# Performance work log

Measured on AMD Instinct MI355X. Metric: run time of the kernel, lower is better.

## Reference

```python
import jax, jax.numpy as jnp
import numpy as np

H = 128          # hidden_dim
OUT = 128        # output_dim
NB = 8           # num_bilinear
NS = 7           # num_spherical
NR = 6           # num_radial
N_BEFORE = 1
N_AFTER = 2
E = 50000        # num_edges
T = 200000       # num_triplets


def _lin_init(key, fan_in, fan_out):
    return jax.random.normal(key, (fan_in, fan_out), jnp.float32) / jnp.sqrt(jnp.float32(fan_in))


def setup_inputs() -> dict:
    key = jax.random.key(0)
    ks = jax.random.split(key, 24)
    inp = {
        "x": jax.random.normal(ks[0], (E, H), jnp.float32),
        "rbf": jax.random.normal(ks[1], (E, NR), jnp.float32),
        "sbf": jax.random.normal(ks[2], (T, NS * NR), jnp.float32),
        "idx_kj": jax.random.randint(ks[3], (T,), 0, E),
        "idx_ji": jax.random.randint(ks[4], (T,), 0, E),
        # params (weights stored [in, out]; y = x @ W + b)
        "W_rbf": _lin_init(ks[5], NR, H),
        "W_sbf": _lin_init(ks[6], NS * NR, NB),
        "Wkj": _lin_init(ks[7], H, H), "bkj": jnp.zeros((H,), jnp.float32),
        "Wji": _lin_init(ks[8], H, H), "bji": jnp.zeros((H,), jnp.float32),
        "Wbil": jax.random.normal(ks[9], (H, NB, H), jnp.float32) * (2.0 / H),
        "before_W1": jax.random.normal(ks[10], (N_BEFORE, H, H), jnp.float32) / jnp.sqrt(jnp.float32(H)),
        "before_b1": jnp.zeros((N_BEFORE, H), jnp.float32),
        "before_W2": jax.random.normal(ks[11], (N_BEFORE, H, H), jnp.float32) / jnp.sqrt(jnp.float32(H)),
        "before_b2": jnp.zeros((N_BEFORE, H), jnp.float32),
        "Wlin": _lin_init(ks[12], H, H), "blin": jnp.zeros((H,), jnp.float32),
        "after_W1": jax.random.normal(ks[13], (N_AFTER, H, H), jnp.float32) / jnp.sqrt(jnp.float32(H)),
        "after_b1": jnp.zeros((N_AFTER, H), jnp.float32),
        "after_W2": jax.random.normal(ks[14], (N_AFTER, H, H), jnp.float32) / jnp.sqrt(jnp.float32(H)),
        "after_b2": jnp.zeros((N_AFTER, H), jnp.float32),
        "Wout": _lin_init(ks[15], H, OUT), "bout": jnp.zeros((OUT,), jnp.float32),
    }
    return inp


def _fwd(x, rbf, sbf, W_rbf, W_sbf, Wkj, bkj, Wji, bji, Wbil,
         before_W1, before_b1, before_W2, before_b2, Wlin, blin,
         after_W1, after_b1, after_W2, after_b2, Wout, bout,
         idx_kj, idx_ji):
    act = jax.nn.silu  # swish
    rbf_h = rbf @ W_rbf                       # [E, H]
    sbf_h = sbf @ W_sbf                       # [T, NB]
    x_ji = act(x @ Wji + bji)                 # [E, H]
    x_kj = act(x @ Wkj + bkj) * rbf_h         # [E, H]
    xg = x_kj[idx_kj]                         # gather -> [T, H]
    # bilinear: out[w,i] = sum_{j,l} sbf_h[w,j] * xg[w,l] * Wbil[i,j,l]
    # loop over the small num_bilinear axis to avoid a [T,H,NB] intermediate
    msg = sbf_h[:, 0:1] * (xg @ Wbil[:, 0, :].T)
    for j in range(1, NB):
        msg = msg + sbf_h[:, j:j + 1] * (xg @ Wbil[:, j, :].T)
    agg = jax.ops.segment_sum(msg, idx_ji, num_segments=x.shape[0])  # scatter-sum [E, H]
    h = x_ji + agg
    for i in range(before_W1.shape[0]):
        h = h + act(act(h @ before_W1[i] + before_b1[i]) @ before_W2[i] + before_b2[i])
    h = act(h @ Wlin + blin) + x
    for i in range(after_W1.shape[0]):
        h = h + act(act(h @ after_W1[i] + after_b1[i]) @ after_W2[i] + after_b2[i])
    return act(h @ Wout + bout)


def reference(x, rbf, sbf, idx_kj, idx_ji, W_rbf, W_sbf, Wkj, bkj, Wji, bji, Wbil,
              before_W1, before_b1, before_W2, before_b2, Wlin, blin,
              after_W1, after_b1, after_W2, after_b2, Wout, bout):
    return _fwd(x, rbf, sbf, W_rbf, W_sbf, Wkj, bkj, Wji, bji, Wbil,
                before_W1, before_b1, before_W2, before_b2, Wlin, blin,
                after_W1, after_b1, after_W2, after_b2, Wout, bout,
                idx_kj, idx_ji)
```

## Files before the change

### kernel.cpp

```cpp
#include <hip/hip_runtime.h>
#include <hip/hip_bf16.h>

#define NEDGE 50000
#define NTRI 200000

typedef __attribute__((ext_vector_type(8))) short short8;
typedef __attribute__((ext_vector_type(4))) short short4v;
typedef __attribute__((ext_vector_type(4))) float f32x4;

__device__ __forceinline__ float silu_f(float v) { return v / (1.0f + __expf(-v)); }

__device__ __forceinline__ short f2bf(float f) {
    unsigned u = __float_as_uint(f);
    unsigned r = (u + 0x7FFFu + ((u >> 16) & 1u)) >> 16;
    return (short)r;
}
__device__ __forceinline__ float bf2f(short s) {
    return __uint_as_float(((unsigned)(unsigned short)s) << 16);
}


__global__ void cvt_kernel(const float* __restrict__ src, short* __restrict__ dst, int n4) {
    int i = blockIdx.x * 256 + threadIdx.x;
    if (i < n4) {
        float4 v = ((const float4*)src)[i];
        short4v o;
        o[0] = f2bf(v.x); o[1] = f2bf(v.y); o[2] = f2bf(v.z); o[3] = f2bf(v.w);
        ((short4v*)dst)[i] = o;
    }
}

struct TP { const float* s[10]; short* d[10]; };
__global__ void t128_all(TP p) {
    const float* __restrict__ src = p.s[blockIdx.y];
    short* __restrict__ dst = p.d[blockIdx.y];
    int i = blockIdx.x * 256 + threadIdx.x;
    int k = i >> 7, n = i & 127;
    dst[n * 128 + k] = f2bf(src[i]);
}

__global__ __launch_bounds__(256) void sbfh_kernel(const float* __restrict__ sbf,
                                                   const float* __restrict__ Wsbf,
                                                   float* __restrict__ out) {
    __shared__ float s[32 * 42];
    __shared__ float w[42 * 8];
    int tid = threadIdx.x;
    size_t base = (size_t)blockIdx.x * 32;
    for (int u = tid; u < 32 * 42; u += 256) s[u] = sbf[base * 42 + u];
    for (int u = tid; u < 42 * 8; u += 256) w[u] = Wsbf[u];
    __syncthreads();
    int row = tid >> 3, j = tid & 7;
    float acc = 0.f;
    #pragma unroll
    for (int k = 0; k < 42; ++k) acc += s[row * 42 + k] * w[k * 8 + j];
    out[base * 8 + tid] = acc;
}


__global__ void hist_kernel(const int* __restrict__ ji, int* __restrict__ counts) {
    int i = blockIdx.x * 256 + threadIdx.x;
    if (i < NTRI) atomicAdd(&counts[ji[i]], 1);
}

__global__ void scan1_kernel(const int* __restrict__ counts, int* __restrict__ partial,
                             int* __restrict__ bsum) {
    __shared__ int tmp[256];
    int tid = threadIdx.x;
    int i = blockIdx.x * 256 + tid;
    int v = (i < NEDGE) ? counts[i] : 0;
    tmp[tid] = v; __syncthreads();
    #pragma unroll
    for (int o = 1; o < 256; o <<= 1) {
        int t = (tid >= o) ? tmp[tid - o] : 0;
        __syncthreads();
        tmp[tid] += t;
        __syncthreads();
    }
    if (i < NEDGE) partial[i] = tmp[tid] - v;
    if (tid == 255) bsum[blockIdx.x] = tmp[255];
}

__global__ void scan2_kernel(int* __restrict__ bsum, int nb) {
    __shared__ int tmp[256];
    int tid = threadIdx.x;
    int v = (tid < nb) ? bsum[tid] : 0;
    tmp[tid] = v; __syncthreads();
    #pragma unroll
    for (int o = 1; o < 256; o <<= 1) {
        int t = (tid >= o) ? tmp[tid - o] : 0;
        __syncthreads();
        tmp[tid] += t;
        __syncthreads();
    }
    if (tid < nb) bsum[tid] = tmp[tid] - v;
}

__global__ void scan3_kernel(const int* __restrict__ partial, const int* __restrict__ bsum,
                             int* __restrict__ rowptr, int* __restrict__ wcur) {
    int i = blockIdx.x * 256 + threadIdx.x;
    if (i < NEDGE) {
        int r = partial[i] + bsum[blockIdx.x];
        rowptr[i] = r;
        wcur[i] = r;
    }
}

__global__ void scatter_kernel(const int* __restrict__ ji, int* __restrict__ wcur,
                               int* __restrict__ perm) {
    int w = blockIdx.x * 256 + threadIdx.x;
    if (w < NTRI) {
        int p = atomicAdd(&wcur[ji[w]], 1);
        perm[p] = w;
    }
}

__global__ void permute_kernel(const int* __restrict__ perm, const int* __restrict__ idx_kj,
                               const float* __restrict__ sbfh, int* __restrict__ kjp,
                               float* __restrict__ sbfhp) {
    int p = blockIdx.x * 256 + threadIdx.x;
    if (p < NTRI) {
        int w = perm[p];
        kjp[p] = idx_kj[w];
        float4 a = *(const float4*)(sbfh + (size_t)w * 8);
        float4 b = *(const float4*)(sbfh + (size_t)w * 8 + 4);
        *(float4*)(sbfhp + (size_t)p * 8) = a;
        *(float4*)(sbfhp + (size_t)p * 8 + 4) = b;
    }
}

#define BE 32
__global__ __launch_bounds__(512) void bilinear_fused(
    const short* __restrict__ xkj, const float* __restrict__ sbfhp,
    const int* __restrict__ kjp, const int* __restrict__ rowptr,
    const int* __restrict__ counts,
    const float* __restrict__ xji, const short* __restrict__ WbT,
    float* __restrict__ h, short* __restrict__ hb)
{
    __shared__ __align__(16) short ylds[BE * 1024];
    __shared__ __align__(16) short blds[128 * 64];

    int tid = threadIdx.x;
    int e0 = blockIdx.x * BE;
    int wv = tid >> 6, lane = tid & 63, g = lane >> 4, ln = lane & 15;

    int eidx = e0 + ((lane < BE) ? lane : BE - 1);
    if (eidx > NEDGE - 1) eidx = NEDGE - 1;
    int rp_l = rowptr[eidx];
    int ct_l = counts[eidx];

    for (int es = 0; es < 4; ++es) {
        int e_loc = wv * 4 + es;
        int e = e0 + e_loc;
        float accA[8], accB[8];
        #pragma unroll
        for (int j = 0; j < 8; ++j) { accA[j] = 0.f; accB[j] = 0.f; }
        if (e < NEDGE) {
            int p0 = __builtin_amdgcn_readfirstlane(__shfl(rp_l, e_loc));
            int n  = __builtin_amdgcn_readfirstlane(__shfl(ct_l, e_loc));
            for (int tc = 0; tc < n; tc += 64) {
                int mm = n - tc; if (mm > 64) mm = 64;
                int li = (lane < mm) ? lane : mm - 1;
                int kt = kjp[p0 + tc + li];
                for (int tb = 0; tb < mm; tb += 4) {
                    int m4 = mm - tb; if (m4 > 4) m4 = 4;
                    int i1 = tb + 1 < mm ? tb + 1 : mm - 1;
                    int i2 = tb + 2 < mm ? tb + 2 : mm - 1;
                    int i3 = tb + 3 < mm ? tb + 3 : mm - 1;
                    int k0 = __shfl(kt, tb), k1 = __shfl(kt, i1);
                    int k2 = __shfl(kt, i2), k3 = __shfl(kt, i3);
                    unsigned xv0 = *(const unsigned*)(xkj + (size_t)k0 * 128 + lane * 2);
                    unsigned xv1 = *(const unsigned*)(xkj + (size_t)k1 * 128 + lane * 2);
                    unsigned xv2 = *(const unsigned*)(xkj + (size_t)k2 * 128 + lane * 2);
                    unsigned xv3 = *(const unsigned*)(xkj + (size_t)k3 * 128 + lane * 2);
                    unsigned xq[4] = {xv0, xv1, xv2, xv3};
                    #pragma unroll
                    for (int s = 0; s < 4; ++s) {
                        if (s < m4) {
                            float x0 = bf2f((short)(xq[s] & 0xffff));
                            float x1 = bf2f((short)(xq[s] >> 16));
                            const float* sp = sbfhp + (size_t)(p0 + tc + tb + s) * 8;
                            #pragma unroll
                            for (int j = 0; j < 8; ++j) {
                                float sv = sp[j];
                                accA[j] += sv * x0; accB[j] += sv * x1;
                            }
                        }
                    }
                }
            }
        }
        unsigned xr = (unsigned)((e_loc & 7) << 4);
        #pragma unroll
        for (int j = 0; j < 8; ++j) {
            unsigned bo = ((unsigned)(e_loc * 2048 + (j * 256 + lane * 4))) ^ xr;
            unsigned pk = (unsigned)(unsigned short)f2bf(accA[j]) |
                          ((unsigned)(unsigned short)f2bf(accB[j]) << 16);
            *(unsigned*)((char*)ylds + bo) = pk;
        }
    }

    int rt = wv >> 2, cq = wv & 3;
    f32x4 acc0 = (f32x4){0.f,0.f,0.f,0.f}, acc1 = (f32x4){0.f,0.f,0.f,0.f};

    short8 wreg0, wreg1;
    {
        int u0 = tid, u1 = tid + 512;
        wreg0 = *(const short8*)(WbT + (size_t)(u0 >> 3) * 1024 + (u0 & 7) * 8);
        wreg1 = *(const short8*)(WbT + (size_t)(u1 >> 3) * 1024 + (u1 & 7) * 8);
    }

    for (int c = 0; c < 16; ++c) {
        __syncthreads();
        {
            int u0 = tid, u1 = tid + 512;
            int bi0 = u0 >> 3, bc0 = u0 & 7;
            int bi1 = u1 >> 3, bc1 = u1 & 7;
            unsigned bo0 = (unsigned)(bi0 * 128 + bc0 * 16) ^ (unsigned)((bi0 & 7) << 4);
            unsigned bo1 = (unsigned)(bi1 * 128 + bc1 * 16) ^ (unsigned)((bi1 & 7) << 4);
            *(short8*)((char*)blds + bo0) = wreg0;
            *(short8*)((char*)blds + bo1) = wreg1;
            if (c < 15) {
                wreg0 = *(const short8*)(WbT + (size_t)bi0 * 1024 + (c + 1) * 64 + bc0 * 8);
                wreg1 = *(const short8*)(WbT + (size_t)bi1 * 1024 + (c + 1) * 64 + bc1 * 8);
            }
        }
        __syncthreads();
        #pragma unroll
        for (int kk = 0; kk < 2; ++kk) {
            int row = rt * 16 + ln;
            unsigned ab = ((unsigned)(row * 2048 + (c * 64 + kk * 32 + g * 8) * 2))
                          ^ ((unsigned)((row & 7) << 4));
            short8 a = *(short8*)((char*)ylds + ab);
            #pragma unroll
            for (int nt = 0; nt < 2; ++nt) {
                int bi = cq * 32 + nt * 16 + ln;
                unsigned bb = ((unsigned)(bi * 128 + kk * 64 + g * 16))
                              ^ ((unsigned)((bi & 7) << 4));
                short8 b = *(short8*)((char*)blds + bb);
                if (nt == 0) acc0 = __builtin_amdgcn_mfma_f32_16x16x32_bf16(a, b, acc0, 0, 0, 0);
                else         acc1 = __builtin_amdgcn_mfma_f32_16x16x32_bf16(a, b, acc1, 0, 0, 0);
            }
        }
    }

    #pragma unroll
    for (int nt = 0; nt < 2; ++nt) {
        int col = cq * 32 + nt * 16 + ln;
        #pragma unroll
        for (int r2 = 0; r2 < 4; ++r2) {
            int e = e0 + rt * 16 + g * 4 + r2;
            if (e < NEDGE) {
                size_t o = (size_t)e * 128 + col;
                float v = (nt == 0 ? acc0[r2] : acc1[r2]) + xji[o];
                h[o] = v; hb[o] = f2bf(v);
            }
        }
    }
}

__global__ __launch_bounds__(256) void gemm_x(
    const short* __restrict__ xb, const short* __restrict__ Wjit,
    const short* __restrict__ Wkjt, const float* __restrict__ bji,
    const float* __restrict__ bkj, const float* __restrict__ rbf,
    const float* __restrict__ Wrbf, float* __restrict__ xji,
    short* __restrict__ xkj)
{
    __shared__ __align__(16) short w1[128 * 128];
    __shared__ __align__(16) short w2[128 * 128];
    int tid = threadIdx.x;
    int wv = tid >> 6, lane = tid & 63, g = lane >> 4, ln = lane & 15;
    int rowBase = blockIdx.x * 64 + wv * 16;

    #pragma unroll
    for (int q = 0; q < 8; ++q) {
        int idx = tid + q * 256;
        int wi = idx >> 4, wc = idx & 15;
        unsigned bo = (unsigned)(wi * 256 + wc * 16) ^ (unsigned)((wi & 7) << 4);
        *(short8*)((char*)w1 + bo) = *(const short8*)(Wjit + wi * 128 + wc * 8);
        *(short8*)((char*)w2 + bo) = *(const short8*)(Wkjt + wi * 128 + wc * 8);
    }

    int arow = rowBase + ln; if (arow > NEDGE - 1) arow = NEDGE - 1;
    const short8* Ar = (const short8*)(xb + (size_t)arow * 128);
    short8 af[4];
    #pragma unroll
    for (int kc = 0; kc < 4; ++kc) af[kc] = Ar[kc * 4 + g];

    __syncthreads();

    f32x4 acc1[8], acc2[8];
    #pragma unroll
    for (int nt = 0; nt < 8; ++nt) {
        acc1[nt] = (f32x4){0.f,0.f,0.f,0.f};
        acc2[nt] = (f32x4){0.f,0.f,0.f,0.f};
    }
    #pragma unroll
    for (int kc = 0; kc < 4; ++kc) {
        #pragma unroll
        for (int nt = 0; nt < 8; ++nt) {
            int wi = nt * 16 + ln;
            unsigned bo = (unsigned)(wi * 256 + kc * 64 + g * 16) ^ (unsigned)((wi & 7) << 4);
            short8 b1 = *(short8*)((char*)w1 + bo);
            short8 b2 = *(short8*)((char*)w2 + bo);
            acc1[nt] = __builtin_amdgcn_mfma_f32_16x16x32_bf16(af[kc], b1, acc1[nt], 0, 0, 0);
            acc2[nt] = __builtin_amdgcn_mfma_f32_16x16x32_bf16(af[kc], b2, acc2[nt], 0, 0, 0);
        }
    }

    #pragma unroll
    for (int r = 0; r < 4; ++r) {
        int row = rowBase + g * 4 + r;
        bool ok = row < NEDGE;
        int crow = ok ? row : NEDGE - 1;
        float rr[6];
        #pragma unroll
        for (int q = 0; q < 6; ++q) rr[q] = rbf[(size_t)crow * 6 + q];
        #pragma unroll
        for (int nt = 0; nt < 8; ++nt) {
            int col = nt * 16 + ln;
            if (ok) {
                size_t o = (size_t)row * 128 + col;
                xji[o] = silu_f(acc1[nt][r] + bji[col]);
                float rb = 0.f;
                #pragma unroll
                for (int q = 0; q < 6; ++q) rb += rr[q] * Wrbf[q * 128 + col];
                xkj[o] = f2bf(silu_f(acc2[nt][r] + bkj[col]) * rb);
            }
        }
    }
}

struct ChainP { const short* W[8]; const float* B[8]; };
__global__ __launch_bounds__(256) void chain_kernel(
    ChainP p, const short* __restrict__ hb, const float* __restrict__ hin,
    const float* __restrict__ x, float* __restrict__ out)
{
    __shared__ __align__(16) short wlds[2][128 * 128];
    __shared__ __align__(16) short actlds[64 * 128];
    int tid = threadIdx.x;
    int wv = tid >> 6, lane = tid & 63, g = lane >> 4, ln = lane & 15;
    int rowBase = blockIdx.x * 64;

    #pragma unroll
    for (int q = 0; q < 8; ++q) {
        int idx = tid + q * 256;
        int wi = idx >> 4, wc = idx & 15;
        unsigned bo = (unsigned)(wi * 256 + wc * 16) ^ (unsigned)((wi & 7) << 4);
        *(short8*)((char*)wlds[0] + bo) = *(const short8*)(p.W[0] + wi * 128 + wc * 8);
    }

    float hreg[8][4];
    #pragma unroll
    for (int nt = 0; nt < 8; ++nt)
        #pragma unroll
        for (int r = 0; r < 4; ++r) {
            int row = rowBase + wv * 16 + g * 4 + r;
            if (row > NEDGE - 1) row = NEDGE - 1;
            hreg[nt][r] = hin[(size_t)row * 128 + nt * 16 + ln];
        }

    int arow = rowBase + wv * 16 + ln; if (arow > NEDGE - 1) arow = NEDGE - 1;
    short8 af[4];
    #pragma unroll
    for (int kc = 0; kc < 4; ++kc)
        af[kc] = *(const short8*)(hb + (size_t)arow * 128 + kc * 32 + g * 8);

    const int modes[8] = {0, 1, 2, 0, 1, 0, 1, 3};

    #pragma unroll
    for (int l = 0; l < 8; ++l) {
        __syncthreads();
        if (l > 0) {
            int ar = wv * 16 + ln;
            unsigned sw = ((unsigned)(ar & 7)) << 4;
            #pragma unroll
            for (int kc = 0; kc < 4; ++kc)
                af[kc] = *(short8*)((char*)actlds +
                          (((unsigned)(ar * 256 + (kc * 32 + g * 8) * 2)) ^ sw));
        }
        __syncthreads();

        f32x4 acc[8];
        #pragma unroll
        for (int nt = 0; nt < 8; ++nt) acc[nt] = (f32x4){0.f,0.f,0.f,0.f};
        #pragma unroll
        for (int kc = 0; kc < 4; ++kc) {
            #pragma unroll
            for (int nt = 0; nt < 8; ++nt) {
                int wi = nt * 16 + ln;
                unsigned bo = (unsigned)(wi * 256 + kc * 64 + g * 16) ^ (unsigned)((wi & 7) << 4);
                short8 b = *(short8*)((char*)wlds[l & 1] + bo);
                acc[nt] = __builtin_amdgcn_mfma_f32_16x16x32_bf16(af[kc], b, acc[nt], 0, 0, 0);
            }
        }

        if (l < 7) {
            #pragma unroll
            for (int q = 0; q < 8; ++q) {
                int idx = tid + q * 256;
                int wi = idx >> 4, wc = idx & 15;
                unsigned bo = (unsigned)(wi * 256 + wc * 16) ^ (unsigned)((wi & 7) << 4);
                *(short8*)((char*)wlds[(l + 1) & 1] + bo) =
                    *(const short8*)(p.W[l + 1] + wi * 128 + wc * 8);
            }
        }

        int mode = modes[l];
        #pragma unroll
        for (int nt = 0; nt < 8; ++nt) {
            int col = nt * 16 + ln;
            float bv = p.B[l][col];
            #pragma unroll
            for (int r = 0; r < 4; ++r) {
                int lrow = wv * 16 + g * 4 + r;
                int row = rowBase + lrow;
                float v = silu_f(acc[nt][r] + bv);
                if (mode == 1) { v += hreg[nt][r]; hreg[nt][r] = v; }
                else if (mode == 2) {
                    int cr = row > NEDGE - 1 ? NEDGE - 1 : row;
                    v += x[(size_t)cr * 128 + col];
                    hreg[nt][r] = v;
                } else if (mode == 3) {
                    if (row < NEDGE) out[(size_t)row * 128 + col] = v;
                }
                if (mode != 3) {
                    unsigned sw2 = ((unsigned)(lrow & 7)) << 4;
                    unsigned bo = ((unsigned)(lrow * 256 + col * 2)) ^ sw2;
                    *(short*)((char*)actlds + bo) = f2bf(v);
                }
            }
        }
    }
}

extern "C" void kernel_launch(void* const* d_in, const int* in_sizes, int n_in,
                              void* d_out, int out_size, void* d_ws, size_t ws_size,
                              hipStream_t stream) {
    const float* x      = (const float*)d_in[0];
    const float* rbf    = (const float*)d_in[1];
    const float* sbf    = (const float*)d_in[2];
    const int*   idx_kj = (const int*)d_in[3];
    const int*   idx_ji = (const int*)d_in[4];
    const float* W_rbf  = (const float*)d_in[5];
    const float* W_sbf  = (const float*)d_in[6];
    const float* Wkj    = (const float*)d_in[7];
    const float* bkj    = (const float*)d_in[8];
    const float* Wji    = (const float*)d_in[9];
    const float* bji    = (const float*)d_in[10];
    const float* Wbil   = (const float*)d_in[11];
    const float* bW1    = (const float*)d_in[12];
    const float* bb1    = (const float*)d_in[13];
    const float* bW2    = (const float*)d_in[14];
    const float* bb2    = (const float*)d_in[15];
    const float* Wlin   = (const float*)d_in[16];
    const float* blin   = (const float*)d_in[17];
    const float* aW1    = (const float*)d_in[18];
    const float* ab1    = (const float*)d_in[19];
    const float* aW2    = (const float*)d_in[20];
    const float* ab2    = (const float*)d_in[21];
    const float* Wout   = (const float*)d_in[22];
    const float* bout   = (const float*)d_in[23];
    float* out = (float*)d_out;

    char* ws = (char*)d_ws;
    size_t off = 0;
    auto alloc = [&](size_t bytes) { char* p = ws + off; off += bytes; return p; };
    short* xb    = (short*)alloc((size_t)NEDGE * 128 * 2);
    short* xkj   = (short*)alloc((size_t)NEDGE * 128 * 2);
    short* hbb   = (short*)alloc((size_t)NEDGE * 128 * 2);
    float* sbfh  = (float*)alloc((size_t)NTRI * 8 * 4);
    float* sbfhp = (float*)alloc(((size_t)NTRI * 8 + 64) * 4);
    float* xji   = (float*)alloc((size_t)NEDGE * 128 * 4);
    float* h     = (float*)alloc((size_t)NEDGE * 128 * 4);
    short* WbT   = (short*)alloc((size_t)131072 * 2);
    short* Wt[10];
    for (int i = 0; i < 10; ++i) Wt[i] = (short*)alloc((size_t)16384 * 2);
    int* counts  = (int*)alloc((size_t)NEDGE * 4);
    int* partial = (int*)alloc((size_t)NEDGE * 4);
    int* rowptr  = (int*)alloc((size_t)NEDGE * 4);
    int* wcur    = (int*)alloc((size_t)NEDGE * 4);
    int* bsum    = (int*)alloc(256 * 4);
    int* perm    = (int*)alloc((size_t)NTRI * 4);
    int* kjp     = (int*)alloc((size_t)(NTRI + 64) * 4);
    (void)ws_size; (void)n_in; (void)in_sizes; (void)out_size;

    hipMemsetAsync(counts, 0, (size_t)NEDGE * 4, stream);

    cvt_kernel<<<dim3((NEDGE * 128 / 4 + 255) / 256), 256, 0, stream>>>(x, xb, NEDGE * 128 / 4);
    cvt_kernel<<<dim3((131072 / 4 + 255) / 256), 256, 0, stream>>>(Wbil, WbT, 131072 / 4);

    TP tp;
    const float* srcs[10] = {Wkj, Wji, bW1, bW2, Wlin, aW1, aW1 + 16384, aW2, aW2 + 16384, Wout};
    for (int i = 0; i < 10; ++i) { tp.s[i] = srcs[i]; tp.d[i] = Wt[i]; }
    t128_all<<<dim3(64, 10), 256, 0, stream>>>(tp);

    sbfh_kernel<<<dim3(NTRI / 32), 256, 0, stream>>>(sbf, W_sbf, sbfh);

    int NB1 = (NEDGE + 255) / 256;
    hist_kernel<<<dim3((NTRI + 255) / 256), 256, 0, stream>>>(idx_ji, counts);
    scan1_kernel<<<dim3(NB1), 256, 0, stream>>>(counts, partial, bsum);
    scan2_kernel<<<dim3(1), 256, 0, stream>>>(bsum, NB1);
    scan3_kernel<<<dim3(NB1), 256, 0, stream>>>(partial, bsum, rowptr, wcur);
    scatter_kernel<<<dim3((NTRI + 255) / 256), 256, 0, stream>>>(idx_ji, wcur, perm);
    permute_kernel<<<dim3((NTRI + 255) / 256), 256, 0, stream>>>(perm, idx_kj, sbfh, kjp, sbfhp);

    int gE = (NEDGE + 63) / 64;
    gemm_x<<<gE, 256, 0, stream>>>(xb, Wt[1], Wt[0], bji, bkj, rbf, W_rbf, xji, xkj);

    bilinear_fused<<<dim3((NEDGE + BE - 1) / BE), 512, 0, stream>>>(
        xkj, sbfhp, kjp, rowptr, counts, xji, WbT, h, hbb);

    ChainP cp;
    cp.W[0] = Wt[2]; cp.B[0] = bb1;
    cp.W[1] = Wt[3]; cp.B[1] = bb2;
    cp.W[2] = Wt[4]; cp.B[2] = blin;
    cp.W[3] = Wt[5]; cp.B[3] = ab1;
    cp.W[4] = Wt[7]; cp.B[4] = ab2;
    cp.W[5] = Wt[6]; cp.B[5] = ab1 + 128;
    cp.W[6] = Wt[8]; cp.B[6] = ab2 + 128;
    cp.W[7] = Wt[9]; cp.B[7] = bout;
    chain_kernel<<<gE, 256, 0, stream>>>(cp, hbb, h, x, out);
}
```

Baseline: 357.7 us.

## Fuse scatter with permute and split chain kernel columns across twice the waves

Merges the scatter and permute kernels so each triplet writes its kj index and sbf_h row straight into its CSR slot, which drops the perm array and one launch. The chain kernel now runs 512 threads, with two waves sharing each 16-row tile and each wave computing half the output columns. It keeps a single LDS weight buffer, prefetching the next layer's weights into registers and writing them to LDS after the barrier. It also initialises the accumulators with the bias and packs bf16 pairs with a lane shuffle into 32-bit LDS stores. The aims are more waves per CU, less LDS use, and fewer kernel launches, at the cost of a less coalesced scattered write of sbf_h and extra register pressure from the prefetched weights.

```diff
diff --git a/kernel.cpp b/kernel.cpp
--- a/kernel.cpp
+++ b/kernel.cpp
@@ -105,21 +105,12 @@
     }
 }
 
-__global__ void scatter_kernel(const int* __restrict__ ji, int* __restrict__ wcur,
-                               int* __restrict__ perm) {
+__global__ void scatter_kernel(const int* __restrict__ ji, const int* __restrict__ idx_kj,
+                               const float* __restrict__ sbfh, int* __restrict__ wcur,
+                               int* __restrict__ kjp, float* __restrict__ sbfhp) {
     int w = blockIdx.x * 256 + threadIdx.x;
     if (w < NTRI) {
         int p = atomicAdd(&wcur[ji[w]], 1);
-        perm[p] = w;
-    }
-}
-
-__global__ void permute_kernel(const int* __restrict__ perm, const int* __restrict__ idx_kj,
-                               const float* __restrict__ sbfh, int* __restrict__ kjp,
-                               float* __restrict__ sbfhp) {
-    int p = blockIdx.x * 256 + threadIdx.x;
-    if (p < NTRI) {
-        int w = perm[p];
         kjp[p] = idx_kj[w];
         float4 a = *(const float4*)(sbfh + (size_t)w * 8);
         float4 b = *(const float4*)(sbfh + (size_t)w * 8 + 4);
@@ -331,47 +322,56 @@
 }
 
 struct ChainP { const short* W[8]; const float* B[8]; };
-__global__ __launch_bounds__(256) void chain_kernel(
+__global__ __launch_bounds__(512, 4) void chain_kernel(
     ChainP p, const short* __restrict__ hb, const float* __restrict__ hin,
     const float* __restrict__ x, float* __restrict__ out)
 {
-    __shared__ __align__(16) short wlds[2][128 * 128];
+    __shared__ __align__(16) short wlds[128 * 128];
     __shared__ __align__(16) short actlds[64 * 128];
     int tid = threadIdx.x;
     int wv = tid >> 6, lane = tid & 63, g = lane >> 4, ln = lane & 15;
+    int rt = wv >> 1, ch = wv & 1;
     int rowBase = blockIdx.x * 64;
 
     #pragma unroll
-    for (int q = 0; q < 8; ++q) {
-        int idx = tid + q * 256;
+    for (int q = 0; q < 4; ++q) {
+        int idx = tid + q * 512;
         int wi = idx >> 4, wc = idx & 15;
         unsigned bo = (unsigned)(wi * 256 + wc * 16) ^ (unsigned)((wi & 7) << 4);
-        *(short8*)((char*)wlds[0] + bo) = *(const short8*)(p.W[0] + wi * 128 + wc * 8);
-    }
-
-    float hreg[8][4];
-    #pragma unroll
-    for (int nt = 0; nt < 8; ++nt)
+        *(short8*)((char*)wlds + bo) = *(const short8*)(p.W[0] + wi * 128 + wc * 8);
+    }
+
+    float hreg[4][4];
+    #pragma unroll
+    for (int nt = 0; nt < 4; ++nt)
         #pragma unroll
         for (int r = 0; r < 4; ++r) {
-            int row = rowBase + wv * 16 + g * 4 + r;
+            int row = rowBase + rt * 16 + g * 4 + r;
             if (row > NEDGE - 1) row = NEDGE - 1;
-            hreg[nt][r] = hin[(size_t)row * 128 + nt * 16 + ln];
-        }
-
-    int arow = rowBase + wv * 16 + ln; if (arow > NEDGE - 1) arow = NEDGE - 1;
+            hreg[nt][r] = hin[(size_t)row * 128 + ch * 64 + nt * 16 + ln];
+        }
+
+    int arow = rowBase + rt * 16 + ln; if (arow > NEDGE - 1) arow = NEDGE - 1;
     short8 af[4];
     #pragma unroll
     for (int kc = 0; kc < 4; ++kc)
         af[kc] = *(const short8*)(hb + (size_t)arow * 128 + kc * 32 + g * 8);
 
+    short8 wreg[4];
     const int modes[8] = {0, 1, 2, 0, 1, 0, 1, 3};
 
     #pragma unroll
     for (int l = 0; l < 8; ++l) {
         __syncthreads();
         if (l > 0) {
-            int ar = wv * 16 + ln;
+            #pragma unroll
+            for (int q = 0; q < 4; ++q) {
+                int idx = tid + q * 512;
+                int wi = idx >> 4, wc = idx & 15;
+                unsigned bo = (unsigned)(wi * 256 + wc * 16) ^ (unsigned)((wi & 7) << 4);
+                *(short8*)((char*)wlds + bo) = wreg[q];
+            }
+            int ar = rt * 16 + ln;
             unsigned sw = ((unsigned)(ar & 7)) << 4;
             #pragma unroll
             for (int kc = 0; kc < 4; ++kc)
@@ -380,41 +380,41 @@
         }
         __syncthreads();
 
-        f32x4 acc[8];
-        #pragma unroll
-        for (int nt = 0; nt < 8; ++nt) acc[nt] = (f32x4){0.f,0.f,0.f,0.f};
+        if (l < 7) {
+            #pragma unroll
+            for (int q = 0; q < 4; ++q) {
+                int idx = tid + q * 512;
+                int wi = idx >> 4, wc = idx & 15;
+                wreg[q] = *(const short8*)(p.W[l + 1] + wi * 128 + wc * 8);
+            }
+        }
+
+        f32x4 acc[4];
+        #pragma unroll
+        for (int nt = 0; nt < 4; ++nt) {
+            float bv = p.B[l][ch * 64 + nt * 16 + ln];
+            acc[nt] = (f32x4){bv, bv, bv, bv};
+        }
         #pragma unroll
         for (int kc = 0; kc < 4; ++kc) {
             #pragma unroll
-            for (int nt = 0; nt < 8; ++nt) {
-                int wi = nt * 16 + ln;
+            for (int nt = 0; nt < 4; ++nt) {
+                int wi = ch * 64 + nt * 16 + ln;
                 unsigned bo = (unsigned)(wi * 256 + kc * 64 + g * 16) ^ (unsigned)((wi & 7) << 4);
-                short8 b = *(short8*)((char*)wlds[l & 1] + bo);
+                short8 b = *(short8*)((char*)wlds + bo);
                 acc[nt] = __builtin_amdgcn_mfma_f32_16x16x32_bf16(af[kc], b, acc[nt], 0, 0, 0);
             }
         }
 
-        if (l < 7) {
-            #pragma unroll
-            for (int q = 0; q < 8; ++q) {
-                int idx = tid + q * 256;
-                int wi = idx >> 4, wc = idx & 15;
-                unsigned bo = (unsigned)(wi * 256 + wc * 16) ^ (unsigned)((wi & 7) << 4);
-                *(short8*)((char*)wlds[(l + 1) & 1] + bo) =
-                    *(const short8*)(p.W[l + 1] + wi * 128 + wc * 8);
-            }
-        }
-
         int mode = modes[l];
         #pragma unroll
-        for (int nt = 0; nt < 8; ++nt) {
-            int col = nt * 16 + ln;
-            float bv = p.B[l][col];
+        for (int nt = 0; nt < 4; ++nt) {
+            int col = ch * 64 + nt * 16 + ln;
             #pragma unroll
             for (int r = 0; r < 4; ++r) {
-                int lrow = wv * 16 + g * 4 + r;
+                int lrow = rt * 16 + g * 4 + r;
                 int row = rowBase + lrow;
-                float v = silu_f(acc[nt][r] + bv);
+                float v = silu_f(acc[nt][r]);
                 if (mode == 1) { v += hreg[nt][r]; hreg[nt][r] = v; }
                 else if (mode == 2) {
                     int cr = row > NEDGE - 1 ? NEDGE - 1 : row;
@@ -424,9 +424,14 @@
                     if (row < NEDGE) out[(size_t)row * 128 + col] = v;
                 }
                 if (mode != 3) {
-                    unsigned sw2 = ((unsigned)(lrow & 7)) << 4;
-                    unsigned bo = ((unsigned)(lrow * 256 + col * 2)) ^ sw2;
-                    *(short*)((char*)actlds + bo) = f2bf(v);
+                    unsigned bits = (unsigned)(unsigned short)f2bf(v);
+                    unsigned other = __shfl_xor((int)bits, 1, 64);
+                    unsigned pk = (ln & 1) ? (other | (bits << 16)) : (bits | (other << 16));
+                    if ((ln & 1) == (r & 1)) {
+                        unsigned bo = ((unsigned)(lrow * 256 + (col & ~1) * 2))
+                                      ^ (((unsigned)(lrow & 7)) << 4);
+                        *(unsigned*)((char*)actlds + bo) = pk;
+                    }
                 }
             }
         }
@@ -480,7 +485,6 @@
     int* rowptr  = (int*)alloc((size_t)NEDGE * 4);
     int* wcur    = (int*)alloc((size_t)NEDGE * 4);
     int* bsum    = (int*)alloc(256 * 4);
-    int* perm    = (int*)alloc((size_t)NTRI * 4);
     int* kjp     = (int*)alloc((size_t)(NTRI + 64) * 4);
     (void)ws_size; (void)n_in; (void)in_sizes; (void)out_size;
 
@@ -501,8 +505,8 @@
     scan1_kernel<<<dim3(NB1), 256, 0, stream>>>(counts, partial, bsum);
     scan2_kernel<<<dim3(1), 256, 0, stream>>>(bsum, NB1);
     scan3_kernel<<<dim3(NB1), 256, 0, stream>>>(partial, bsum, rowptr, wcur);
-    scatter_kernel<<<dim3((NTRI + 255) / 256), 256, 0, stream>>>(idx_ji, wcur, perm);
-    permute_kernel<<<dim3((NTRI + 255) / 256), 256, 0, stream>>>(perm, idx_kj, sbfh, kjp, sbfhp);
+    scatter_kernel<<<dim3((NTRI + 255) / 256), 256, 0, stream>>>(idx_ji, idx_kj, sbfh,
+                                                                 wcur, kjp, sbfhp);
 
     int gE = (NEDGE + 63) / 64;
     gemm_x<<<gE, 256, 0, stream>>>(xb, Wt[1], Wt[0], bji, bkj, rbf, W_rbf, xji, xkj);
@@ -519,5 +523,5 @@
     cp.W[5] = Wt[6]; cp.B[5] = ab1 + 128;
     cp.W[6] = Wt[8]; cp.B[6] = ab2 + 128;
     cp.W[7] = Wt[9]; cp.B[7] = bout;
-    chain_kernel<<<gE, 256, 0, stream>>>(cp, hbb, h, x, out);
-}
+    chain_kernel<<<gE, 512, 0, stream>>>(cp, hbb, h, x, out);
+}
```

After: 352.2 us. About the same (-1.5%).
